# Optimization experiments

Hardware: AMD Instinct MI355X
Metric: run time of the kernel (lower is better)

## Reference

```python
import jax, jax.numpy as jnp
import numpy as np

N_NODES = 8192
N_EDGES = 262144
N_REL = 8
NUM_CLASSES = 151
EMB = 256
BOX = 1024
HID = 512
OUT = 256
N_TASKS = 2


def setup_inputs() -> dict:
    key = jax.random.key(0)
    ks = jax.random.split(key, 20)
    w = lambda k, shape: jax.random.normal(k, shape, dtype=jnp.float32) * 0.02
    return {
        "box_features": jax.random.normal(ks[0], (N_NODES, BOX), dtype=jnp.float32),
        "pred_labels": jax.random.randint(ks[1], (N_NODES,), 0, NUM_CLASSES),
        "edge_index": jax.random.randint(ks[2], (2, N_EDGES), 0, N_NODES),
        "edge_type": jax.random.randint(ks[3], (N_EDGES,), 0, N_REL),
        "nodes_per_graph": 128,
        "emb_table": w(ks[4], (NUM_CLASSES, EMB)),
        "W_lin": w(ks[5], (BOX + EMB, HID)),
        "b_lin": jnp.zeros((HID,), jnp.float32),
        "rel_W1": w(ks[6], (N_REL, HID, HID)),
        "root_W1": w(ks[7], (HID, HID)),
        "b1": jnp.zeros((HID,), jnp.float32),
        "rel_W2": w(ks[8], (N_REL, HID, OUT)),
        "root_W2": w(ks[9], (HID, OUT)),
        "b2": jnp.zeros((OUT,), jnp.float32),
        "Wc1": w(ks[10], (OUT, OUT)),
        "bc1": jnp.zeros((OUT,), jnp.float32),
        "Wc2": w(ks[11], (OUT, N_TASKS)),
        "bc2": jnp.zeros((N_TASKS,), jnp.float32),
    }


def rgcn_conv(x, src, dst, etype, rel_W, root_W, b):
    """PyG RGCNConv: per-relation mean aggregation + root weight + bias."""
    R, _, out_dim = rel_W.shape
    N = x.shape[0]
    transformed = jnp.einsum('ni,rio->rno', x, rel_W)      # [R, N, out]
    msg = transformed[etype, src]                           # [E, out] gather per edge
    seg = etype * N + dst                                   # (relation, dst) segment id
    sums = jax.ops.segment_sum(msg, seg, num_segments=R * N)
    cnt = jax.ops.segment_sum(jnp.ones((msg.shape[0],), x.dtype), seg, num_segments=R * N)
    mean = sums / jnp.maximum(cnt, 1.0)[:, None]
    agg = mean.reshape(R, N, out_dim).sum(0)                # sum over relations
    return agg + x @ root_W + b


def reference(box_features, pred_labels, edge_index, edge_type, nodes_per_graph,
              emb_table, W_lin, b_lin, rel_W1, root_W1, b1, rel_W2, root_W2, b2,
              Wc1, bc1, Wc2, bc2):
    src, dst = edge_index[0], edge_index[1]
    # obj embedding + concat with box features
    x = jnp.concatenate([box_features, emb_table[pred_labels]], axis=-1)  # [N, 1280]
    x = x @ W_lin + b_lin                                                  # [N, 512]
    x = jax.nn.relu(rgcn_conv(x, src, dst, edge_type, rel_W1, root_W1, b1))
    x = rgcn_conv(x, src, dst, edge_type, rel_W2, root_W2, b2)             # [N, 256]
    # mean graph pooling over equal-size graphs
    B = x.shape[0] // nodes_per_graph
    pooled = x.reshape(B, nodes_per_graph, -1).mean(axis=1)                # [B, 256]
    # classifier (dropout is identity in eval)
    y_logits = (pooled @ Wc1 + bc1) @ Wc2 + bc2                            # [B, n_tasks]
    y_prob = jax.nn.softmax(y_logits, axis=-1)
    return y_logits, y_prob
```

## Files before the change

### kernel.cpp

```cpp
#include <hip/hip_runtime.h>
#include <cstdint>

#define NNODES 8192
#define NEDGES 262144
#define NRELS  8
#define EMBD   256
#define BOXD   1024
#define HIDD   512
#define OUTD   256
#define NSEG   (NRELS * NNODES)
#define K0DIM  (BOXD + EMBD)
#define KSDIM  (NRELS * HIDD + HIDD)

using bf16x8 = __attribute__((ext_vector_type(8))) short;
using f32x4  = __attribute__((ext_vector_type(4))) float;
using us4    = __attribute__((ext_vector_type(4))) unsigned short;

__device__ __forceinline__ unsigned short f2b(float f) {
    union { float f; uint32_t u; } v; v.f = f;
    uint32_t r = v.u + 0x7FFFu + ((v.u >> 16) & 1u);
    return (unsigned short)(r >> 16);
}

__device__ __forceinline__ us4 cvt4(f32x4 v) {
    us4 u;
    u[0] = f2b(v[0]); u[1] = f2b(v[1]); u[2] = f2b(v[2]); u[3] = f2b(v[3]);
    return u;
}

__device__ __forceinline__ float b2f_lo(uint32_t w) {
    union { uint32_t u; float f; } v; v.u = w << 16; return v.f;
}
__device__ __forceinline__ float b2f_hi(uint32_t w) {
    union { uint32_t u; float f; } v; v.u = w & 0xffff0000u; return v.f;
}

__global__ void k_build_x0(const float* __restrict__ box, const int* __restrict__ labels,
                           const float* __restrict__ emb, unsigned short* __restrict__ X0) {
    int n = blockIdx.x;
    int lab = labels[n];
    const f32x4* b = (const f32x4*)(box + (size_t)n * BOXD);
    const f32x4* e = (const f32x4*)(emb + (size_t)lab * EMBD);
    us4* o = (us4*)(X0 + (size_t)n * K0DIM);
    for (int j = threadIdx.x; j < K0DIM / 4; j += 256) {
        f32x4 v = (j < BOXD / 4) ? b[j] : e[j - BOXD / 4];
        o[j] = cvt4(v);
    }
}

__global__ void k_transpose_all(const float* __restrict__ W_lin, const float* __restrict__ rel_W1,
                                const float* __restrict__ root_W1, const float* __restrict__ rel_W2,
                                const float* __restrict__ root_W2,
                                unsigned short* __restrict__ W0t, unsigned short* __restrict__ W1t,
                                unsigned short* __restrict__ W2t) {
    __shared__ float t[32][33];
    int bid = blockIdx.x;
    const float* src; unsigned short* dst; int No, ld, kOff, kb, ob;
    if (bid < 640)        { int g = bid;        src = W_lin;   dst = W0t; No = 512; ld = K0DIM; kOff = 0;    kb = g % 40;  ob = g / 40; }
    else if (bid < 2688)  { int g = bid - 640;  src = rel_W1;  dst = W1t; No = 512; ld = KSDIM; kOff = 0;    kb = g % 128; ob = g / 128; }
    else if (bid < 2944)  { int g = bid - 2688; src = root_W1; dst = W1t; No = 512; ld = KSDIM; kOff = 4096; kb = g % 16;  ob = g / 16; }
    else if (bid < 3968)  { int g = bid - 2944; src = rel_W2;  dst = W2t; No = 256; ld = KSDIM; kOff = 0;    kb = g % 128; ob = g / 128; }
    else                  { int g = bid - 3968; src = root_W2; dst = W2t; No = 256; ld = KSDIM; kOff = 4096; kb = g % 16;  ob = g / 16; }
    int kt = kb * 32, ot = ob * 32;
    int tx = threadIdx.x & 31, ty = threadIdx.x >> 5;
#pragma unroll
    for (int i = 0; i < 4; i++) {
        int k = kt + ty + i * 8;
        t[ty + i * 8][tx] = src[(size_t)k * No + ot + tx];
    }
    __syncthreads();
#pragma unroll
    for (int i = 0; i < 4; i++) {
        int o = ot + ty + i * 8;
        dst[(size_t)o * ld + kOff + kt + tx] = f2b(t[tx][ty + i * 8]);
    }
}

__global__ void k_hist(const int* __restrict__ etype, const int* __restrict__ edst,
                       int* __restrict__ cnt) {
    int e = blockIdx.x * 256 + threadIdx.x;
    if (e >= NEDGES) return;
    atomicAdd(&cnt[etype[e] * NNODES + edst[e]], 1);
}

__global__ __launch_bounds__(1024) void k_scan(const int* __restrict__ cnt,
                                               int* __restrict__ segstart) {
    __shared__ int part[1024];
    __shared__ int sup[16];
    __shared__ int supx[16];
    int t = threadIdx.x;
    int base = t * 64;
    int s = 0;
    for (int i = 0; i < 64; i++) s += cnt[base + i];
    part[t] = s;
    __syncthreads();
    if (t < 16) {
        int a = 0;
        for (int i = 0; i < 64; i++) a += part[t * 64 + i];
        sup[t] = a;
    }
    __syncthreads();
    if (t == 0) {
        int a = 0;
        for (int i = 0; i < 16; i++) { supx[i] = a; a += sup[i]; }
    }
    __syncthreads();
    int a = supx[t >> 6];
    for (int i = (t & ~63); i < t; i++) a += part[i];
    for (int i = 0; i < 64; i++) { segstart[base + i] = a; a += cnt[base + i]; }
    if (t == 1023) segstart[NSEG] = a;
}

__global__ void k_scatter(const int* __restrict__ etype, const int* __restrict__ esrc,
                          const int* __restrict__ edst, const int* __restrict__ segstart,
                          int* __restrict__ cursor, int* __restrict__ esorted) {
    int e = blockIdx.x * 256 + threadIdx.x;
    if (e >= NEDGES) return;
    int key = etype[e] * NNODES + edst[e];
    int pos = atomicAdd(&cursor[key], 1);
    esorted[segstart[key] + pos] = esrc[e];
}

__global__ __launch_bounds__(256) void k_aggregate(
        const unsigned short* __restrict__ x, const int* __restrict__ segstart,
        const int* __restrict__ esorted, unsigned short* __restrict__ Xin) {
    int seg = blockIdx.x * 4 + (threadIdx.x >> 6);
    int lane = threadIdx.x & 63;
    int r = seg >> 13;
    int dstn = seg & (NNODES - 1);
    float a[8] = {0, 0, 0, 0, 0, 0, 0, 0};
    float b[8] = {0, 0, 0, 0, 0, 0, 0, 0};
    int s0 = segstart[seg], s1 = segstart[seg + 1];
    int t = s0;
    for (; t + 2 <= s1; t += 2) {
        uint4 v0 = *(const uint4*)(x + (size_t)esorted[t] * HIDD + lane * 8);
        uint4 v1 = *(const uint4*)(x + (size_t)esorted[t + 1] * HIDD + lane * 8);
        a[0] += b2f_lo(v0.x); a[1] += b2f_hi(v0.x);
        a[2] += b2f_lo(v0.y); a[3] += b2f_hi(v0.y);
        a[4] += b2f_lo(v0.z); a[5] += b2f_hi(v0.z);
        a[6] += b2f_lo(v0.w); a[7] += b2f_hi(v0.w);
        b[0] += b2f_lo(v1.x); b[1] += b2f_hi(v1.x);
        b[2] += b2f_lo(v1.y); b[3] += b2f_hi(v1.y);
        b[4] += b2f_lo(v1.z); b[5] += b2f_hi(v1.z);
        b[6] += b2f_lo(v1.w); b[7] += b2f_hi(v1.w);
    }
    if (t < s1) {
        uint4 v0 = *(const uint4*)(x + (size_t)esorted[t] * HIDD + lane * 8);
        a[0] += b2f_lo(v0.x); a[1] += b2f_hi(v0.x);
        a[2] += b2f_lo(v0.y); a[3] += b2f_hi(v0.y);
        a[4] += b2f_lo(v0.z); a[5] += b2f_hi(v0.z);
        a[6] += b2f_lo(v0.w); a[7] += b2f_hi(v0.w);
    }
    float iv = (s1 > s0) ? (1.0f / (float)(s1 - s0)) : 1.0f;
#pragma unroll
    for (int j = 0; j < 8; j++) a[j] = (a[j] + b[j]) * iv;
    uint4 u;
    u.x = (uint32_t)f2b(a[0]) | ((uint32_t)f2b(a[1]) << 16);
    u.y = (uint32_t)f2b(a[2]) | ((uint32_t)f2b(a[3]) << 16);
    u.z = (uint32_t)f2b(a[4]) | ((uint32_t)f2b(a[5]) << 16);
    u.w = (uint32_t)f2b(a[6]) | ((uint32_t)f2b(a[7]) << 16);
    *(uint4*)(Xin + (size_t)dstn * KSDIM + r * HIDD + lane * 8) = u;
}

__global__ __launch_bounds__(256) void k_aggpool(
        const unsigned short* __restrict__ x, const int* __restrict__ segstart,
        const int* __restrict__ esorted, float* __restrict__ PXp) {
    int b = blockIdx.x;
    int q = b & 3, r = (b >> 2) & 7, g = b >> 5;
    int wave = threadIdx.x >> 6, lane = threadIdx.x & 63;
    float a[8] = {0, 0, 0, 0, 0, 0, 0, 0};
    int segbase = r * NNODES + g * 128 + q * 32 + wave * 8;
#pragma unroll 1
    for (int i = 0; i < 8; ++i) {
        int s0 = segstart[segbase + i], s1 = segstart[segbase + i + 1];
        if (s0 == s1) continue;
        float p[8] = {0, 0, 0, 0, 0, 0, 0, 0};
        for (int t = s0; t < s1; ++t) {
            uint4 v = *(const uint4*)(x + (size_t)esorted[t] * HIDD + lane * 8);
            p[0] += b2f_lo(v.x); p[1] += b2f_hi(v.x);
            p[2] += b2f_lo(v.y); p[3] += b2f_hi(v.y);
            p[4] += b2f_lo(v.z); p[5] += b2f_hi(v.z);
            p[6] += b2f_lo(v.w); p[7] += b2f_hi(v.w);
        }
        float w = 1.0f / (128.0f * (float)(s1 - s0));
#pragma unroll
        for (int j = 0; j < 8; j++) a[j] += p[j] * w;
    }
    __shared__ float red[4][512];
#pragma unroll
    for (int j = 0; j < 8; j++) red[wave][lane * 8 + j] = a[j];
    __syncthreads();
    for (int c = threadIdx.x; c < 512; c += 256) {
        float s = red[0][c] + red[1][c] + red[2][c] + red[3][c];
        PXp[((size_t)q * 64 + g) * KSDIM + r * 512 + c] = s;
    }
}

__global__ __launch_bounds__(256) void k_rootpool(
        const unsigned short* __restrict__ x, float* __restrict__ PXp) {
    int g = blockIdx.x >> 2, q = blockIdx.x & 3;
    int wave = threadIdx.x >> 6, lane = threadIdx.x & 63;
    float a[8] = {0, 0, 0, 0, 0, 0, 0, 0};
    int n0 = g * 128 + q * 32 + wave * 8;
#pragma unroll
    for (int i = 0; i < 8; ++i) {
        uint4 v = *(const uint4*)(x + (size_t)(n0 + i) * HIDD + lane * 8);
        a[0] += b2f_lo(v.x); a[1] += b2f_hi(v.x);
        a[2] += b2f_lo(v.y); a[3] += b2f_hi(v.y);
        a[4] += b2f_lo(v.z); a[5] += b2f_hi(v.z);
        a[6] += b2f_lo(v.w); a[7] += b2f_hi(v.w);
    }
    __shared__ float red[4][512];
#pragma unroll
    for (int j = 0; j < 8; j++) red[wave][lane * 8 + j] = a[j];
    __syncthreads();
    for (int c = threadIdx.x; c < 512; c += 256) {
        float s = red[0][c] + red[1][c] + red[2][c] + red[3][c];
        PXp[((size_t)q * 64 + g) * KSDIM + 4096 + c] = s * (1.0f / 128.0f);
    }
}

__global__ __launch_bounds__(512, 4) void k_gemm(
        const unsigned short* __restrict__ A,
        const unsigned short* __restrict__ Bt,
        float* __restrict__ P,
        int M, int N, int K, int Kc) {
    __shared__ unsigned short As[2][128 * 64];
    __shared__ unsigned short Bs[2][128 * 64];
    const int tid = threadIdx.x;
    const int lane = tid & 63, wid = tid >> 6;
    const int tiles_m = M >> 7;
    const int tm = blockIdx.x % tiles_m, tn = blockIdx.x / tiles_m;
    const int m0 = tm << 7, n0 = tn << 7;
    const int wr = wid >> 2, wc = wid & 3;
    const int k0 = blockIdx.y * Kc;

    f32x4 acc[4][2];
#pragma unroll
    for (int i = 0; i < 4; i++)
#pragma unroll
        for (int j = 0; j < 2; j++) acc[i][j] = (f32x4){0.f, 0.f, 0.f, 0.f};

    const int rowg = tid >> 3;
    const int srcc = (tid & 7) ^ (rowg & 7);
    const unsigned short* gA = A  + (size_t)(m0 + rowg) * K + k0 + srcc * 8;
    const unsigned short* gB = Bt + (size_t)(n0 + rowg) * K + k0 + srcc * 8;
    const int ldsbase = wid * 512;

    auto stage = [&](int bsel, int kt) {
#pragma unroll
        for (int i = 0; i < 2; ++i) {
            __builtin_amdgcn_global_load_lds(
                (const __attribute__((address_space(1))) void*)(gA + kt + i * 64 * K),
                (__attribute__((address_space(3))) void*)&As[bsel][i * 4096 + ldsbase], 16, 0, 0);
            __builtin_amdgcn_global_load_lds(
                (const __attribute__((address_space(1))) void*)(gB + kt + i * 64 * K),
                (__attribute__((address_space(3))) void*)&Bs[bsel][i * 4096 + ldsbase], 16, 0, 0);
        }
    };

    const int arow = wr * 64 + (lane & 15);
    const int brow = wc * 32 + (lane & 15);
    const int l7 = lane & 7;
    const int c0 = lane >> 4;

    const int nt = Kc >> 6;
    int cur = 0;
    stage(0, 0);
    asm volatile("s_waitcnt vmcnt(0)" ::: "memory");
    __builtin_amdgcn_s_barrier();

    for (int t = 0; t < nt; ++t) {
        if (t + 1 < nt) stage(cur ^ 1, (t + 1) * 64);
#pragma unroll
        for (int s4 = 0; s4 < 2; ++s4) {
            const int slot = (c0 + s4 * 4) ^ l7;
            bf16x8 af[4], bfr[2];
#pragma unroll
            for (int m = 0; m < 4; m++)
                af[m] = *(const bf16x8*)&As[cur][(arow + m * 16) * 64 + slot * 8];
#pragma unroll
            for (int n = 0; n < 2; n++)
                bfr[n] = *(const bf16x8*)&Bs[cur][(brow + n * 16) * 64 + slot * 8];
#pragma unroll
            for (int m = 0; m < 4; m++)
#pragma unroll
                for (int n = 0; n < 2; n++)
                    acc[m][n] = __builtin_amdgcn_mfma_f32_16x16x32_bf16(af[m], bfr[n], acc[m][n], 0, 0, 0);
        }
        if (t + 1 < nt) {
            asm volatile("s_waitcnt vmcnt(0)" ::: "memory");
            __builtin_amdgcn_s_barrier();
            cur ^= 1;
        }
    }

    float* Pout = P + (size_t)blockIdx.y * M * N;
    const int crow0 = m0 + wr * 64 + (lane >> 4) * 4;
    const int ccol0 = n0 + wc * 32 + (lane & 15);
#pragma unroll
    for (int n = 0; n < 2; n++) {
        int col = ccol0 + n * 16;
#pragma unroll
        for (int m = 0; m < 4; m++)
#pragma unroll
            for (int r = 0; r < 4; r++)
                Pout[(size_t)(crow0 + m * 16 + r) * N + col] = acc[m][n][r];
    }
}

template <int RELU, int WROOT>
__global__ void k_reduce_bf(const float* __restrict__ P, const float* __restrict__ bias,
                            unsigned short* __restrict__ xbf, unsigned short* __restrict__ Xin,
                            int MN) {
    int idx = (blockIdx.x * 256 + threadIdx.x) * 4;
    f32x4 v = *(const f32x4*)&P[idx];
    v += *(const f32x4*)&P[(size_t)MN + idx];
    v += *(const f32x4*)&bias[idx & 511];
    if (RELU) {
#pragma unroll
        for (int j = 0; j < 4; j++) v[j] = fmaxf(v[j], 0.f);
    }
    us4 u = cvt4(v);
    *(us4*)&xbf[idx] = u;
    if (WROOT) {
        int row = idx >> 9, col = idx & 511;
        *(us4*)&Xin[(size_t)row * KSDIM + NRELS * HIDD + col] = u;
    }
}

__global__ void k_head1(const float* __restrict__ PXp, const unsigned short* __restrict__ W2t,
                        const float* __restrict__ b2, float* __restrict__ pooled) {
    __shared__ float red[4][64];
    int g = blockIdx.x >> 2;
    int ob = (blockIdx.x & 3) * 64;
    int ol = threadIdx.x & 63, kq = threadIdx.x >> 6;
    const float* p0 = PXp + ((size_t)0 * 64 + g) * KSDIM + kq * 1152;
    const float* p1 = PXp + ((size_t)1 * 64 + g) * KSDIM + kq * 1152;
    const float* p2 = PXp + ((size_t)2 * 64 + g) * KSDIM + kq * 1152;
    const float* p3 = PXp + ((size_t)3 * 64 + g) * KSDIM + kq * 1152;
    const unsigned short* w = W2t + (size_t)(ob + ol) * KSDIM + kq * 1152;
    float s = 0.f;
    for (int k = 0; k < 1152; k += 8) {
        uint4 wv = *(const uint4*)(w + k);
        float pk[8];
#pragma unroll
        for (int j = 0; j < 8; j++) pk[j] = p0[k + j] + p1[k + j] + p2[k + j] + p3[k + j];
        s += pk[0] * b2f_lo(wv.x) + pk[1] * b2f_hi(wv.x)
           + pk[2] * b2f_lo(wv.y) + pk[3] * b2f_hi(wv.y)
           + pk[4] * b2f_lo(wv.z) + pk[5] * b2f_hi(wv.z)
           + pk[6] * b2f_lo(wv.w) + pk[7] * b2f_hi(wv.w);
    }
    red[kq][ol] = s;
    __syncthreads();
    if (threadIdx.x < 64) {
        float t = red[0][threadIdx.x] + red[1][threadIdx.x]
                + red[2][threadIdx.x] + red[3][threadIdx.x];
        pooled[g * 256 + ob + threadIdx.x] = t + b2[ob + threadIdx.x];
    }
}

__global__ void k_head2(const float* __restrict__ pooled, const float* __restrict__ Wc1,
                        const float* __restrict__ bc1, const float* __restrict__ Wc2,
                        const float* __restrict__ bc2, float* __restrict__ out) {
    __shared__ float p[256];
    __shared__ float h[256];
    __shared__ float lg[2];
    int b = blockIdx.x, o = threadIdx.x;
    p[o] = pooled[b * 256 + o];
    __syncthreads();
    float s1 = bc1[o];
    for (int i = 0; i < 256; i++) s1 += p[i] * Wc1[i * 256 + o];
    h[o] = s1;
    __syncthreads();
    if (o < 2) {
        float t = bc2[o];
        for (int i = 0; i < 256; i++) t += h[i] * Wc2[i * 2 + o];
        lg[o] = t;
        out[b * 2 + o] = t;
    }
    __syncthreads();
    if (o == 0) {
        float m = fmaxf(lg[0], lg[1]);
        float e0 = expf(lg[0] - m), e1 = expf(lg[1] - m);
        float inv = 1.0f / (e0 + e1);
        out[128 + b * 2 + 0] = e0 * inv;
        out[128 + b * 2 + 1] = e1 * inv;
    }
}

extern "C" void kernel_launch(void* const* d_in, const int* in_sizes, int n_in,
                              void* d_out, int out_size, void* d_ws, size_t ws_size,
                              hipStream_t stream) {
    const float* box     = (const float*)d_in[0];
    const int*   labels  = (const int*)d_in[1];
    const int*   eidx    = (const int*)d_in[2];
    const int*   etype   = (const int*)d_in[3];
    const float* emb     = (const float*)d_in[5];
    const float* W_lin   = (const float*)d_in[6];
    const float* b_lin   = (const float*)d_in[7];
    const float* rel_W1  = (const float*)d_in[8];
    const float* root_W1 = (const float*)d_in[9];
    const float* b1      = (const float*)d_in[10];
    const float* rel_W2  = (const float*)d_in[11];
    const float* root_W2 = (const float*)d_in[12];
    const float* b2      = (const float*)d_in[13];
    const float* Wc1     = (const float*)d_in[14];
    const float* bc1     = (const float*)d_in[15];
    const float* Wc2     = (const float*)d_in[16];
    const float* bc2     = (const float*)d_in[17];
    const int* esrc = eidx;
    const int* edst = eidx + NEDGES;

    char* ws = (char*)d_ws;
    size_t off = 0;
    auto alloc = [&](size_t bytes) -> char* {
        char* p = ws + off;
        off += (bytes + 255) & ~(size_t)255;
        return p;
    };
    float* Pp = (float*)alloc((size_t)2 * NNODES * HIDD * 4);
    unsigned short* Xin = (unsigned short*)alloc((size_t)NNODES * KSDIM * 2);
    unsigned short* X0  = Xin;
    unsigned short* xbf = (unsigned short*)alloc((size_t)NNODES * HIDD * 2);
    unsigned short* W0t = (unsigned short*)alloc((size_t)HIDD * K0DIM * 2);
    unsigned short* W1t = (unsigned short*)alloc((size_t)HIDD * KSDIM * 2);
    unsigned short* W2t = (unsigned short*)alloc((size_t)OUTD * KSDIM * 2);
    float* PXp    = (float*)alloc((size_t)4 * 64 * KSDIM * 4);
    float* pooled = (float*)alloc((size_t)64 * OUTD * 4);
    int*   cnt     = (int*)alloc((size_t)NSEG * 4);
    int*   cursor  = (int*)alloc((size_t)NSEG * 4);
    int*   segst   = (int*)alloc((size_t)(NSEG + 1) * 4);
    int*   esorted = (int*)alloc((size_t)NEDGES * 4);
    if (off > ws_size) return;

    float* out = (float*)d_out;
    const int MN = NNODES * HIDD;

    hipMemsetAsync(cnt, 0, (size_t)2 * NSEG * 4, stream);
    k_build_x0<<<NNODES, 256, 0, stream>>>(box, labels, emb, X0);
    k_transpose_all<<<4096, 256, 0, stream>>>(W_lin, rel_W1, root_W1, rel_W2, root_W2,
                                              W0t, W1t, W2t);
    k_hist<<<NEDGES / 256, 256, 0, stream>>>(etype, edst, cnt);
    k_scan<<<1, 1024, 0, stream>>>(cnt, segst);
    k_scatter<<<NEDGES / 256, 256, 0, stream>>>(etype, esrc, edst, segst, cursor, esorted);

    k_gemm<<<dim3((NNODES / 128) * (HIDD / 128), 2), 512, 0, stream>>>(
        X0, W0t, Pp, NNODES, HIDD, K0DIM, K0DIM / 2);
    k_reduce_bf<0, 1><<<MN / 1024, 256, 0, stream>>>(Pp, b_lin, xbf, Xin, MN);

    k_aggregate<<<NSEG / 4, 256, 0, stream>>>(xbf, segst, esorted, Xin);
    k_gemm<<<dim3((NNODES / 128) * (HIDD / 128), 2), 512, 0, stream>>>(
        Xin, W1t, Pp, NNODES, HIDD, KSDIM, KSDIM / 2);
    k_reduce_bf<1, 0><<<MN / 1024, 256, 0, stream>>>(Pp, b1, xbf, Xin, MN);

    k_aggpool<<<2048, 256, 0, stream>>>(xbf, segst, esorted, PXp);
    k_rootpool<<<256, 256, 0, stream>>>(xbf, PXp);
    k_head1<<<256, 256, 0, stream>>>(PXp, W2t, b2, pooled);
    k_head2<<<64, 256, 0, stream>>>(pooled, Wc1, bc1, Wc2, bc2, out);
}
```

Baseline: 299.6 us.

## Fold layer-2 weights and linear classifier into a single 4608x2 projection

Because the second RGCN layer, pooling and the two-layer classifier are all linear, the weights are pre-multiplied (rel_W2/root_W2 times Wc1 times Wc2) into a 4608x2 matrix with a folded bias. Pooled features then project directly to logits in one small kernel. This removes the rel_W2/root_W2 transpose, the head1 matvec and head2, but adds two small weight-precomputation kernels, one of them single-block and serial. Summation order changes, so rounding differs slightly.

```diff
diff --git a/kernel.cpp b/kernel.cpp
--- a/kernel.cpp
+++ b/kernel.cpp
@@ -49,18 +49,14 @@
 }
 
 __global__ void k_transpose_all(const float* __restrict__ W_lin, const float* __restrict__ rel_W1,
-                                const float* __restrict__ root_W1, const float* __restrict__ rel_W2,
-                                const float* __restrict__ root_W2,
-                                unsigned short* __restrict__ W0t, unsigned short* __restrict__ W1t,
-                                unsigned short* __restrict__ W2t) {
+                                const float* __restrict__ root_W1,
+                                unsigned short* __restrict__ W0t, unsigned short* __restrict__ W1t) {
     __shared__ float t[32][33];
     int bid = blockIdx.x;
     const float* src; unsigned short* dst; int No, ld, kOff, kb, ob;
     if (bid < 640)        { int g = bid;        src = W_lin;   dst = W0t; No = 512; ld = K0DIM; kOff = 0;    kb = g % 40;  ob = g / 40; }
     else if (bid < 2688)  { int g = bid - 640;  src = rel_W1;  dst = W1t; No = 512; ld = KSDIM; kOff = 0;    kb = g % 128; ob = g / 128; }
-    else if (bid < 2944)  { int g = bid - 2688; src = root_W1; dst = W1t; No = 512; ld = KSDIM; kOff = 4096; kb = g % 16;  ob = g / 16; }
-    else if (bid < 3968)  { int g = bid - 2944; src = rel_W2;  dst = W2t; No = 256; ld = KSDIM; kOff = 0;    kb = g % 128; ob = g / 128; }
-    else                  { int g = bid - 3968; src = root_W2; dst = W2t; No = 256; ld = KSDIM; kOff = 4096; kb = g % 16;  ob = g / 16; }
+    else                  { int g = bid - 2688; src = root_W1; dst = W1t; No = 512; ld = KSDIM; kOff = 4096; kb = g % 16;  ob = g / 16; }
     int kt = kb * 32, ot = ob * 32;
     int tx = threadIdx.x & 31, ty = threadIdx.x >> 5;
 #pragma unroll
@@ -74,6 +70,45 @@
         int o = ot + ty + i * 8;
         dst[(size_t)o * ld + kOff + kt + tx] = f2b(t[tx][ty + i * 8]);
     }
+}
+
+__global__ void k_wc12(const float* __restrict__ Wc1, const float* __restrict__ bc1,
+                       const float* __restrict__ Wc2, const float* __restrict__ bc2,
+                       const float* __restrict__ b2, float* __restrict__ Wsmall,
+                       float* __restrict__ bbig) {
+    __shared__ float r0[256], r1[256];
+    int i = threadIdx.x;
+    float w0 = 0.f, w1 = 0.f;
+    for (int o = 0; o < 256; o++) {
+        float c = Wc1[i * 256 + o];
+        w0 += c * Wc2[o * 2 + 0];
+        w1 += c * Wc2[o * 2 + 1];
+    }
+    Wsmall[i * 2 + 0] = w0;
+    Wsmall[i * 2 + 1] = w1;
+    r0[i] = b2[i] * w0 + bc1[i] * Wc2[i * 2 + 0];
+    r1[i] = b2[i] * w1 + bc1[i] * Wc2[i * 2 + 1];
+    __syncthreads();
+    for (int s = 128; s > 0; s >>= 1) {
+        if (i < s) { r0[i] += r0[i + s]; r1[i] += r1[i + s]; }
+        __syncthreads();
+    }
+    if (i == 0) { bbig[0] = r0[0] + bc2[0]; bbig[1] = r1[0] + bc2[1]; }
+}
+
+__global__ void k_wbig(const float* __restrict__ rel_W2, const float* __restrict__ root_W2,
+                       const float* __restrict__ Wsmall, float* __restrict__ Wbig) {
+    int k = blockIdx.x * 256 + threadIdx.x;
+    const float* row = (k < 4096) ? rel_W2 + (size_t)k * 256
+                                  : root_W2 + (size_t)(k - 4096) * 256;
+    float s0 = 0.f, s1 = 0.f;
+    for (int o = 0; o < 256; o++) {
+        float v = row[o];
+        s0 += v * Wsmall[o * 2 + 0];
+        s1 += v * Wsmall[o * 2 + 1];
+    }
+    Wbig[k * 2 + 0] = s0;
+    Wbig[k * 2 + 1] = s1;
 }
 
 __global__ void k_hist(const int* __restrict__ etype, const int* __restrict__ edst,
@@ -329,63 +364,37 @@
     }
 }
 
-__global__ void k_head1(const float* __restrict__ PXp, const unsigned short* __restrict__ W2t,
-                        const float* __restrict__ b2, float* __restrict__ pooled) {
-    __shared__ float red[4][64];
-    int g = blockIdx.x >> 2;
-    int ob = (blockIdx.x & 3) * 64;
-    int ol = threadIdx.x & 63, kq = threadIdx.x >> 6;
-    const float* p0 = PXp + ((size_t)0 * 64 + g) * KSDIM + kq * 1152;
-    const float* p1 = PXp + ((size_t)1 * 64 + g) * KSDIM + kq * 1152;
-    const float* p2 = PXp + ((size_t)2 * 64 + g) * KSDIM + kq * 1152;
-    const float* p3 = PXp + ((size_t)3 * 64 + g) * KSDIM + kq * 1152;
-    const unsigned short* w = W2t + (size_t)(ob + ol) * KSDIM + kq * 1152;
-    float s = 0.f;
-    for (int k = 0; k < 1152; k += 8) {
-        uint4 wv = *(const uint4*)(w + k);
-        float pk[8];
-#pragma unroll
-        for (int j = 0; j < 8; j++) pk[j] = p0[k + j] + p1[k + j] + p2[k + j] + p3[k + j];
-        s += pk[0] * b2f_lo(wv.x) + pk[1] * b2f_hi(wv.x)
-           + pk[2] * b2f_lo(wv.y) + pk[3] * b2f_hi(wv.y)
-           + pk[4] * b2f_lo(wv.z) + pk[5] * b2f_hi(wv.z)
-           + pk[6] * b2f_lo(wv.w) + pk[7] * b2f_hi(wv.w);
-    }
-    red[kq][ol] = s;
-    __syncthreads();
-    if (threadIdx.x < 64) {
-        float t = red[0][threadIdx.x] + red[1][threadIdx.x]
-                + red[2][threadIdx.x] + red[3][threadIdx.x];
-        pooled[g * 256 + ob + threadIdx.x] = t + b2[ob + threadIdx.x];
-    }
-}
-
-__global__ void k_head2(const float* __restrict__ pooled, const float* __restrict__ Wc1,
-                        const float* __restrict__ bc1, const float* __restrict__ Wc2,
-                        const float* __restrict__ bc2, float* __restrict__ out) {
-    __shared__ float p[256];
-    __shared__ float h[256];
-    __shared__ float lg[2];
-    int b = blockIdx.x, o = threadIdx.x;
-    p[o] = pooled[b * 256 + o];
-    __syncthreads();
-    float s1 = bc1[o];
-    for (int i = 0; i < 256; i++) s1 += p[i] * Wc1[i * 256 + o];
-    h[o] = s1;
-    __syncthreads();
-    if (o < 2) {
-        float t = bc2[o];
-        for (int i = 0; i < 256; i++) t += h[i] * Wc2[i * 2 + o];
-        lg[o] = t;
-        out[b * 2 + o] = t;
-    }
-    __syncthreads();
-    if (o == 0) {
-        float m = fmaxf(lg[0], lg[1]);
-        float e0 = expf(lg[0] - m), e1 = expf(lg[1] - m);
+__global__ void k_logits(const float* __restrict__ PXp, const float* __restrict__ Wbig,
+                         const float* __restrict__ bbig, float* __restrict__ out) {
+    __shared__ float r0[256], r1[256];
+    int g = blockIdx.x, tid = threadIdx.x;
+    const float* p0 = PXp + ((size_t)0 * 64 + g) * KSDIM;
+    const float* p1 = PXp + ((size_t)1 * 64 + g) * KSDIM;
+    const float* p2 = PXp + ((size_t)2 * 64 + g) * KSDIM;
+    const float* p3 = PXp + ((size_t)3 * 64 + g) * KSDIM;
+    float s0 = 0.f, s1 = 0.f;
+#pragma unroll
+    for (int i = 0; i < 18; i++) {
+        int k = i * 256 + tid;
+        float px = p0[k] + p1[k] + p2[k] + p3[k];
+        s0 += px * Wbig[k * 2 + 0];
+        s1 += px * Wbig[k * 2 + 1];
+    }
+    r0[tid] = s0; r1[tid] = s1;
+    __syncthreads();
+    for (int s = 128; s > 0; s >>= 1) {
+        if (tid < s) { r0[tid] += r0[tid + s]; r1[tid] += r1[tid + s]; }
+        __syncthreads();
+    }
+    if (tid == 0) {
+        float l0 = r0[0] + bbig[0], l1 = r1[0] + bbig[1];
+        out[g * 2 + 0] = l0;
+        out[g * 2 + 1] = l1;
+        float m = fmaxf(l0, l1);
+        float e0 = expf(l0 - m), e1 = expf(l1 - m);
         float inv = 1.0f / (e0 + e1);
-        out[128 + b * 2 + 0] = e0 * inv;
-        out[128 + b * 2 + 1] = e1 * inv;
+        out[128 + g * 2 + 0] = e0 * inv;
+        out[128 + g * 2 + 1] = e1 * inv;
     }
 }
 
@@ -425,9 +434,10 @@
     unsigned short* xbf = (unsigned short*)alloc((size_t)NNODES * HIDD * 2);
     unsigned short* W0t = (unsigned short*)alloc((size_t)HIDD * K0DIM * 2);
     unsigned short* W1t = (unsigned short*)alloc((size_t)HIDD * KSDIM * 2);
-    unsigned short* W2t = (unsigned short*)alloc((size_t)OUTD * KSDIM * 2);
     float* PXp    = (float*)alloc((size_t)4 * 64 * KSDIM * 4);
-    float* pooled = (float*)alloc((size_t)64 * OUTD * 4);
+    float* Wsmall = (float*)alloc((size_t)256 * 2 * 4);
+    float* Wbig   = (float*)alloc((size_t)KSDIM * 2 * 4);
+    float* bbig   = (float*)alloc(2 * 4);
     int*   cnt     = (int*)alloc((size_t)NSEG * 4);
     int*   cursor  = (int*)alloc((size_t)NSEG * 4);
     int*   segst   = (int*)alloc((size_t)(NSEG + 1) * 4);
@@ -439,8 +449,9 @@
 
     hipMemsetAsync(cnt, 0, (size_t)2 * NSEG * 4, stream);
     k_build_x0<<<NNODES, 256, 0, stream>>>(box, labels, emb, X0);
-    k_transpose_all<<<4096, 256, 0, stream>>>(W_lin, rel_W1, root_W1, rel_W2, root_W2,
-                                              W0t, W1t, W2t);
+    k_transpose_all<<<2944, 256, 0, stream>>>(W_lin, rel_W1, root_W1, W0t, W1t);
+    k_wc12<<<1, 256, 0, stream>>>(Wc1, bc1, Wc2, bc2, b2, Wsmall, bbig);
+    k_wbig<<<KSDIM / 256, 256, 0, stream>>>(rel_W2, root_W2, Wsmall, Wbig);
     k_hist<<<NEDGES / 256, 256, 0, stream>>>(etype, edst, cnt);
     k_scan<<<1, 1024, 0, stream>>>(cnt, segst);
     k_scatter<<<NEDGES / 256, 256, 0, stream>>>(etype, esrc, edst, segst, cursor, esorted);
@@ -456,6 +467,5 @@
 
     k_aggpool<<<2048, 256, 0, stream>>>(xbf, segst, esorted, PXp);
     k_rootpool<<<256, 256, 0, stream>>>(xbf, PXp);
-    k_head1<<<256, 256, 0, stream>>>(PXp, W2t, b2, pooled);
-    k_head2<<<64, 256, 0, stream>>>(pooled, Wc1, bc1, Wc2, bc2, out);
-}
+    k_logits<<<64, 256, 0, stream>>>(PXp, Wbig, bbig, out);
+}
```

Result: faster. 255.4 us, median of 2 (-14.8%).
